# Optimization experiments

Measured on AMD Instinct MI355X. Metric: run time of the kernel, lower is better.

The kernel has to match this reference:

```python
import jax, jax.numpy as jnp
import numpy as np

LEAK = 0.01  # torch F.leaky_relu default slope


def _conv1d(x, W, b):
    # x: [B, Cin, L], W: [Cout, Cin, K] -> [B, Cout, L-K+1]
    y = jax.lax.conv_general_dilated(x, W, window_strides=(1,), padding='VALID',
                                     dimension_numbers=('NCH', 'OIH', 'NCH'))
    return y + b[None, :, None]


def _maxpool3(x):
    # MaxPool1d(kernel=3, stride=3, padding=1); torch pads with -inf
    return jax.lax.reduce_window(x, -jnp.inf, jax.lax.max,
                                 (1, 1, 3), (1, 1, 3),
                                 ((0, 0), (0, 0), (1, 1)))


def _lrelu(x):
    return jnp.where(x >= 0, x, LEAK * x)


def _lstm_layer(x, Wih, Whh, b):
    # x: [B, T, D]; Wih: [4H, D]; Whh: [4H, H]; b: [4H]  (torch gate order i,f,g,o)
    B = x.shape[0]
    H = Whh.shape[1]

    def step(carry, xt):
        h, c = carry
        gates = xt @ Wih.T + h @ Whh.T + b  # [B, 4H]
        i, f, g, o = jnp.split(gates, 4, axis=-1)
        c = jax.nn.sigmoid(f) * c + jax.nn.sigmoid(i) * jnp.tanh(g)
        h = jax.nn.sigmoid(o) * jnp.tanh(c)
        return (h, c), h

    init = (jnp.zeros((B, H), x.dtype), jnp.zeros((B, H), x.dtype))
    _, ys = jax.lax.scan(step, init, jnp.swapaxes(x, 0, 1))
    return jnp.swapaxes(ys, 0, 1)  # [B, T, H]


def _lstm3(x, Wih_s, Whh_s, b_s):
    # 3-layer LSTM (dropout=0 in eval); return h_n[-1] + h_n[-2]
    h_last = []
    for l in range(3):
        x = _lstm_layer(x, Wih_s[l], Whh_s[l], b_s[l])
        h_last.append(x[:, -1])
    return h_last[-1] + h_last[-2]


def _forward(data_in, W1, b1, W2, b2, W3, b3,
             fWih, fWhh, fb, tWih, tWhh, tb,
             L1W, L1b, L2W, L2b, L3W, L3b, L4W, L4b):
    T, F, L, P = data_in.shape
    x = data_in.reshape(T * F, L, P).swapaxes(1, 2)  # [B, 3, L]
    x = _maxpool3(_lrelu(_conv1d(x, W1, b1)))  # [B, 10, 170]
    x = _maxpool3(_lrelu(_conv1d(x, W2, b2)))  # [B, 5, 56]
    x = _maxpool3(_lrelu(_conv1d(x, W3, b3)))  # [B, 10, 18]
    x = x.swapaxes(1, 2)                       # [B, 18, 10] packet vectors
    fv = _lstm3(x, fWih, fWhh, fb)             # [B, 10] flow vectors
    fv = fv.reshape(T, F, -1)                  # [T, F, 10]
    tv = _lstm3(fv, tWih, tWhh, tb)            # [T, 10] trace vectors
    h = _lrelu(tv @ L1W.T + L1b)
    h = _lrelu(h @ L2W.T + L2b)
    h = _lrelu(h @ L3W.T + L3b)
    return h @ L4W.T + L4b                     # [T, 7]


def setup_inputs() -> dict:
    key = jax.random.key(0)
    ks = iter(jax.random.split(key, 32))
    n = lambda shape: jax.random.normal(next(ks), shape, dtype=jnp.float32)
    return {
        'data_in': n((64, 64, 512, 3)),
        'W1': n((10, 3, 5)), 'b1': n((10,)),
        'W2': n((5, 10, 5)), 'b2': n((5,)),
        'W3': n((10, 5, 5)), 'b3': n((10,)),
        'fWih': n((3, 40, 10)), 'fWhh': n((3, 40, 10)), 'fb': n((3, 40)),
        'tWih': n((3, 40, 10)), 'tWhh': n((3, 40, 10)), 'tb': n((3, 40)),
        'L1W': n((128, 10)), 'L1b': n((128,)),
        'L2W': n((256, 128)), 'L2b': n((256,)),
        'L3W': n((64, 256)), 'L3b': n((64,)),
        'L4W': n((7, 64)), 'L4b': n((7,)),
    }


def reference(data_in, W1, b1, W2, b2, W3, b3,
              fWih, fWhh, fb, tWih, tWhh, tb,
              L1W, L1b, L2W, L2b, L3W, L3b, L4W, L4b):
    return _forward(data_in, W1, b1, W2, b2, W3, b3,
                    fWih, fWhh, fb, tWih, tWhh, tb,
                    L1W, L1b, L2W, L2b, L3W, L3b, L4W, L4b)
```

## Files before the change

### kernel.cpp

```cpp
#include <hip/hip_runtime.h>
#include <math.h>

#define LEAK 0.01f

typedef float v2f __attribute__((ext_vector_type(2)));

__device__ __forceinline__ float lrelu(float x) { return fmaxf(x, LEAK * x); }
__device__ __forceinline__ float fast_rcp(float x) { return __builtin_amdgcn_rcpf(x); }
__device__ __forceinline__ float sigmoid_f(float x) {
    return fast_rcp(1.0f + exp2f(-1.44269504f * x));
}
__device__ __forceinline__ float tanh_f(float x) {
    return 2.0f * fast_rcp(1.0f + exp2f(-2.88539008f * x)) - 1.0f;
}
__device__ __forceinline__ float readlane_f(float v, int l) {
    return __int_as_float(__builtin_amdgcn_readlane(__float_as_int(v), l));
}

#define DECL5(p) v2f p##_0, p##_1, p##_2, p##_3, p##_4
#define LOAD5(p, src) do { const v2f* _s5 = (const v2f*)(src); \
    p##_0 = _s5[0]; p##_1 = _s5[1]; p##_2 = _s5[2]; p##_3 = _s5[3]; p##_4 = _s5[4]; } while (0)
#define CP5(d, s) do { d##_0 = s##_0; d##_1 = s##_1; d##_2 = s##_2; d##_3 = s##_3; d##_4 = s##_4; } while (0)
#define ZERO5(p) do { p##_0 = (v2f){0.f,0.f}; p##_1 = (v2f){0.f,0.f}; p##_2 = (v2f){0.f,0.f}; \
    p##_3 = (v2f){0.f,0.f}; p##_4 = (v2f){0.f,0.f}; } while (0)
#define DOT5(w, x) ((w##_0 * x##_0 + w##_1 * x##_1) + (w##_2 * x##_2 + w##_3 * x##_3) + w##_4 * x##_4)

#define DECLU(u) float u##0, u##1, u##2, u##3, u##4, u##5, u##6, u##7, u##8, u##9
#define ZEROU(u) do { u##0=u##1=u##2=u##3=u##4=u##5=u##6=u##7=u##8=u##9=0.0f; } while (0)
#define RL10(u, v) do { \
    u##0 = readlane_f(v, 0); u##1 = readlane_f(v, 1); u##2 = readlane_f(v, 2); \
    u##3 = readlane_f(v, 3); u##4 = readlane_f(v, 4); u##5 = readlane_f(v, 5); \
    u##6 = readlane_f(v, 6); u##7 = readlane_f(v, 7); u##8 = readlane_f(v, 8); \
    u##9 = readlane_f(v, 9); } while (0)
#define DOTU(w, u) (fmaf(w##_0.x, u##0, fmaf(w##_0.y, u##1, fmaf(w##_1.x, u##2, fmaf(w##_1.y, u##3, w##_2.x * u##4)))) \
                  + fmaf(w##_2.y, u##5, fmaf(w##_3.x, u##6, fmaf(w##_3.y, u##7, fmaf(w##_4.x, u##8, w##_4.y * u##9)))))

#define L1C 508
#define L1P 170
#define L2C 166
#define L2P 56
#define L3C 52
#define L3P 18
#define TT 18

__global__ __launch_bounds__(256, 4) void conv_kernel(
    const float* __restrict__ in,
    const float* __restrict__ W1, const float* __restrict__ b1,
    const float* __restrict__ W2, const float* __restrict__ b2,
    const float* __restrict__ W3, const float* __restrict__ b3,
    float* __restrict__ xseq)
{
    __shared__ __align__(16) float xsraw[24 + 1536 + 24];
    __shared__ __align__(16) float y1raw[16 + L1P * 10 + 32];
    __shared__ __align__(16) float y2raw[8 + L2P * 6 + 24];
    float* xs = xsraw + 24;
    float* y1 = y1raw + 16;
    float* y2 = y2raw + 8;

    const int tid = threadIdx.x;
    const int b = blockIdx.x;

    {
        const float4* src = (const float4*)(in + (size_t)b * 1536);
        float4* dst4 = (float4*)xs;
        for (int i = tid; i < 384; i += 256) dst4[i] = src[i];
    }
    __syncthreads();

    {
        const int co = tid % 10;
        const int ob = tid / 10;
        if (tid < 250) {
            float w[15];
            #pragma unroll
            for (int q = 0; q < 15; ++q) w[q] = W1[co * 15 + q];
            const float bias = b1[co];
            const int o0 = ob * 7;
            int sb = 3 * o0 - 1;
            float win[21];
            #pragma unroll
            for (int q = 0; q < 21; ++q) win[q] = xs[3 * sb + q];
            #pragma unroll
            for (int r = 0; r < 7; ++r) {
                const int o = o0 + r;
                if (o < L1P) {
                    float a0 = bias, a1 = bias, a2 = bias;
                    #pragma unroll
                    for (int p = 0; p < 3; ++p) {
                        #pragma unroll
                        for (int k = 0; k < 5; ++k) {
                            const float wv = w[p * 5 + k];
                            a0 = fmaf(wv, win[3 * k + p], a0);
                            a1 = fmaf(wv, win[3 * (k + 1) + p], a1);
                            a2 = fmaf(wv, win[3 * (k + 2) + p], a2);
                        }
                    }
                    float best = -3.0e38f;
                    if (sb >= 0)        best = fmaxf(best, lrelu(a0));
                    best = fmaxf(best, lrelu(a1));
                    if (sb + 2 < L1C)   best = fmaxf(best, lrelu(a2));
                    y1[o * 10 + co] = best;
                }
                if (r < 6 && o + 1 < L1P) {
                    #pragma unroll
                    for (int q = 0; q < 12; ++q) win[q] = win[q + 9];
                    #pragma unroll
                    for (int q = 0; q < 9; ++q) win[12 + q] = xs[3 * sb + 21 + q];
                    sb += 3;
                }
            }
        }
    }
    __syncthreads();

    {
        const int co = tid % 5;
        const int ob = tid / 5;
        v2f wv2[25];
        #pragma unroll
        for (int c2 = 0; c2 < 5; ++c2)
            #pragma unroll
            for (int k = 0; k < 5; ++k)
                wv2[c2 * 5 + k] = (v2f){W2[co * 50 + (2 * c2) * 5 + k],
                                        W2[co * 50 + (2 * c2 + 1) * 5 + k]};
        const float bias = b2[co];
        if (tid < 255) {
            for (int r = 0; r < 2; ++r) {
                const int o = ob + 51 * r;
                if (o < L2P) {
                    const int t0 = 3 * o - 1;
                    v2f v0 = {0.f, 0.f}, v1 = {0.f, 0.f}, v2 = {0.f, 0.f};
                    #pragma unroll
                    for (int m = 0; m < 7; ++m) {
                        v2f rows5[5];
                        const v2f* pr = (const v2f*)(y1 + (t0 + m) * 10);
                        #pragma unroll
                        for (int c2 = 0; c2 < 5; ++c2) rows5[c2] = pr[c2];
                        #pragma unroll
                        for (int c2 = 0; c2 < 5; ++c2) {
                            if (m < 5)            v0 += wv2[c2 * 5 + m] * rows5[c2];
                            if (m >= 1 && m <= 5) v1 += wv2[c2 * 5 + m - 1] * rows5[c2];
                            if (m >= 2)           v2 += wv2[c2 * 5 + m - 2] * rows5[c2];
                        }
                    }
                    const float a0 = bias + v0.x + v0.y;
                    const float a1 = bias + v1.x + v1.y;
                    const float a2 = bias + v2.x + v2.y;
                    float best = -3.0e38f;
                    if (t0 >= 0)        best = fmaxf(best, lrelu(a0));
                    best = fmaxf(best, lrelu(a1));
                    if (t0 + 2 < L2C)   best = fmaxf(best, lrelu(a2));
                    y2[o * 6 + co] = best;
                }
            }
        }
    }
    __syncthreads();

    {
        const int co = tid % 10;
        const int o = tid / 10;
        if (o < L3P) {
            v2f wv3[10];
            float ws3[5];
            #pragma unroll
            for (int c2 = 0; c2 < 2; ++c2)
                #pragma unroll
                for (int k = 0; k < 5; ++k)
                    wv3[c2 * 5 + k] = (v2f){W3[co * 25 + (2 * c2) * 5 + k],
                                            W3[co * 25 + (2 * c2 + 1) * 5 + k]};
            #pragma unroll
            for (int k = 0; k < 5; ++k) ws3[k] = W3[co * 25 + 20 + k];
            const float bias = b3[co];
            const int t0 = 3 * o - 1;
            v2f v0 = {0.f, 0.f}, v1 = {0.f, 0.f}, v2 = {0.f, 0.f};
            float s0 = 0.f, s1 = 0.f, s2 = 0.f;
            #pragma unroll
            for (int m = 0; m < 7; ++m) {
                const float* base = y2 + (t0 + m) * 6;
                v2f ra0 = ((const v2f*)base)[0];
                v2f ra1 = ((const v2f*)base)[1];
                float rcm = base[4];
                if (m < 5) {
                    v0 += wv3[m] * ra0; v0 += wv3[5 + m] * ra1;
                    s0 = fmaf(ws3[m], rcm, s0);
                }
                if (m >= 1 && m <= 5) {
                    v1 += wv3[m - 1] * ra0; v1 += wv3[5 + m - 1] * ra1;
                    s1 = fmaf(ws3[m - 1], rcm, s1);
                }
                if (m >= 2) {
                    v2 += wv3[m - 2] * ra0; v2 += wv3[5 + m - 2] * ra1;
                    s2 = fmaf(ws3[m - 2], rcm, s2);
                }
            }
            const float a0 = bias + s0 + v0.x + v0.y;
            const float a1 = bias + s1 + v1.x + v1.y;
            const float a2 = bias + s2 + v2.x + v2.y;
            float best = -3.0e38f;
            if (t0 >= 0)        best = fmaxf(best, lrelu(a0));
            best = fmaxf(best, lrelu(a1));
            if (t0 + 2 < L3C)   best = fmaxf(best, lrelu(a2));
            xseq[(size_t)b * 180 + o * 10 + co] = best;
        }
    }
}

__global__ __launch_bounds__(256, 2) void flow_lstm_kernel(
    const float* __restrict__ xseq,
    const float* __restrict__ fWih, const float* __restrict__ fWhh,
    const float* __restrict__ fb,
    float* __restrict__ fv)
{
    __shared__ __align__(16) float sbuf[3][16 * 18 * 10];
    const int tid = threadIdx.x;
    const int blk = blockIdx.x;

    {
        const float* src = xseq + (size_t)blk * 2880;
        for (int i = tid; i < 2880; i += 256) sbuf[0][i] = src[i];
    }
    __syncthreads();

    const int el = tid >> 4;
    const int j = tid & 15;
    const int jj = (j < 10) ? j : 0;
    const int base = el * 180;
    const int lane = tid & 63;
    const int gbase = lane & 48;

    float fv_acc = 0.0f;

    for (int l = 0; l < 3; ++l) {
        const float* Wi = fWih + l * 400;
        const float* Wh = fWhh + l * 400;
        const float* bb = fb + l * 40;
        DECL5(wii); DECL5(wif); DECL5(wig); DECL5(wio);
        DECL5(whi); DECL5(whf); DECL5(whg); DECL5(who);
        LOAD5(wii, Wi + jj * 10);
        LOAD5(wif, Wi + (10 + jj) * 10);
        LOAD5(wig, Wi + (20 + jj) * 10);
        LOAD5(wio, Wi + (30 + jj) * 10);
        LOAD5(whi, Wh + jj * 10);
        LOAD5(whf, Wh + (10 + jj) * 10);
        LOAD5(whg, Wh + (20 + jj) * 10);
        LOAD5(who, Wh + (30 + jj) * 10);
        const float bi = bb[jj], bf = bb[10 + jj], bg = bb[20 + jj], bo = bb[30 + jj];

        const float* inb = sbuf[l];
        float* outb = sbuf[(l + 1) % 3];
        float c = 0.0f, hj = 0.0f;
        DECL5(hv); ZERO5(hv);
        DECL5(xc); DECL5(xn);
        LOAD5(xc, inb + base);

        for (int t = 0; t < TT; ++t) {
            if (t + 1 < TT) LOAD5(xn, inb + base + (t + 1) * 10);
            v2f ti_ = DOT5(wii, xc) + DOT5(whi, hv);
            v2f tf_ = DOT5(wif, xc) + DOT5(whf, hv);
            v2f tg_ = DOT5(wig, xc) + DOT5(whg, hv);
            v2f to_ = DOT5(wio, xc) + DOT5(who, hv);
            const float ai = sigmoid_f(bi + ti_.x + ti_.y);
            const float af = sigmoid_f(bf + tf_.x + tf_.y);
            const float ag = tanh_f(bg + tg_.x + tg_.y);
            const float ao = sigmoid_f(bo + to_.x + to_.y);
            c = af * c + ai * ag;
            hj = ao * tanh_f(c);
            if (j < 10) outb[base + t * 10 + j] = hj;
            hv_0 = (v2f){__shfl(hj, gbase + 0), __shfl(hj, gbase + 1)};
            hv_1 = (v2f){__shfl(hj, gbase + 2), __shfl(hj, gbase + 3)};
            hv_2 = (v2f){__shfl(hj, gbase + 4), __shfl(hj, gbase + 5)};
            hv_3 = (v2f){__shfl(hj, gbase + 6), __shfl(hj, gbase + 7)};
            hv_4 = (v2f){__shfl(hj, gbase + 8), __shfl(hj, gbase + 9)};
            CP5(xc, xn);
        }
        if (l >= 1) fv_acc += hj;
        __asm__ __volatile__("" ::: "memory");
    }
    if (j < 10) fv[(size_t)(blk * 16 + el) * 10 + j] = fv_acc;
}

__global__ __launch_bounds__(64, 1) void trace_mlp_kernel(
    const float* __restrict__ fv,
    const float* __restrict__ tWih, const float* __restrict__ tWhh,
    const float* __restrict__ tb,
    const float* __restrict__ L1W, const float* __restrict__ L1b,
    const float* __restrict__ L2W, const float* __restrict__ L2b,
    const float* __restrict__ L3W, const float* __restrict__ L3b,
    const float* __restrict__ L4W, const float* __restrict__ L4b,
    float* __restrict__ out)
{
    __shared__ __align__(16) float xrow[640];
    __shared__ __align__(16) float m1[128];
    __shared__ __align__(16) float m2b[256];
    __shared__ __align__(16) float m3[64];

    const int lane = threadIdx.x;
    const int ti = blockIdx.x;

    {
        const float4* src = (const float4*)(fv + (size_t)ti * 640);
        float4* dst = (float4*)xrow;
        for (int i = lane; i < 160; i += 64) dst[i] = src[i];
    }
    __asm__ __volatile__("" ::: "memory");

    const int gt = lane / 10;
    const bool isg = (gt == 2);
    const float m2g = isg ? 2.0f : 1.0f;
    const float am = isg ? 2.0f : 1.0f;
    const float ab = isg ? -1.0f : 0.0f;

    const int r = (lane < 40) ? lane : 0;
    DECL5(wi0); DECL5(wh0); DECL5(wi1); DECL5(wh1); DECL5(wi2); DECL5(wh2);
    LOAD5(wi0, tWih + r * 10);
    LOAD5(wh0, tWhh + r * 10);
    LOAD5(wi1, tWih + 400 + r * 10);
    LOAD5(wh1, tWhh + 400 + r * 10);
    LOAD5(wi2, tWih + 800 + r * 10);
    LOAD5(wh2, tWhh + 800 + r * 10);
    const float bs0 = tb[r], bs1 = tb[40 + r], bs2 = tb[80 + r];

    DECLU(u0); DECLU(u1); DECLU(u2);
    ZEROU(u0); ZEROU(u1); ZEROU(u2);
    float c0 = 0.0f, c1 = 0.0f, c2 = 0.0f;
    DECL5(xc); DECL5(xn);

#define TICK(D0, D1, D2) do { \
    float g0_ = 0.f, g1_ = 0.f, g2_ = 0.f; \
    if (D2) g2_ = bs2 + DOTU(wi2, u1) + DOTU(wh2, u2); \
    if (D1) g1_ = bs1 + DOTU(wi1, u0) + DOTU(wh1, u1); \
    if (D0) { v2f ax_ = DOT5(wi0, xc); g0_ = bs0 + ax_.x + ax_.y + DOTU(wh0, u0); } \
    float a0_ = 0.f, a1_ = 0.f, a2_ = 0.f; \
    if (D2) a2_ = am * sigmoid_f(m2g * g2_) + ab; \
    if (D1) a1_ = am * sigmoid_f(m2g * g1_) + ab; \
    if (D0) a0_ = am * sigmoid_f(m2g * g0_) + ab; \
    float f2_ = 0.f, q2_ = 0.f, o2_ = 0.f; \
    float f1_ = 0.f, q1_ = 0.f, o1_ = 0.f; \
    float f0_ = 0.f, q0_ = 0.f, o0_ = 0.f; \
    if (D2) { f2_ = __shfl(a2_, lane + 10); q2_ = __shfl(a2_, lane + 20); o2_ = __shfl(a2_, lane + 30); } \
    if (D1) { f1_ = __shfl(a1_, lane + 10); q1_ = __shfl(a1_, lane + 20); o1_ = __shfl(a1_, lane + 30); } \
    if (D0) { f0_ = __shfl(a0_, lane + 10); q0_ = __shfl(a0_, lane + 20); o0_ = __shfl(a0_, lane + 30); } \
    if (D2) { c2 = f2_ * c2 + a2_ * q2_; float h_ = o2_ * tanh_f(c2); RL10(u2, h_); } \
    if (D1) { c1 = f1_ * c1 + a1_ * q1_; float h_ = o1_ * tanh_f(c1); RL10(u1, h_); } \
    if (D0) { c0 = f0_ * c0 + a0_ * q0_; float h_ = o0_ * tanh_f(c0); RL10(u0, h_); } \
} while (0)

    LOAD5(xc, xrow + 0);
    LOAD5(xn, xrow + 10);
    TICK(true, false, false); CP5(xc, xn);
    LOAD5(xn, xrow + 20);
    TICK(true, true, false); CP5(xc, xn);
    for (int tau = 2; tau < 63; ++tau) {
        LOAD5(xn, xrow + (tau + 1) * 10);
        TICK(true, true, true);
        CP5(xc, xn);
    }
    TICK(true, true, true);
    TICK(false, true, true);
    TICK(false, false, true);
#undef TICK

    DECLU(tv);
    tv0 = u10 + u20; tv1 = u11 + u21; tv2 = u12 + u22; tv3 = u13 + u23;
    tv4 = u14 + u24; tv5 = u15 + u25; tv6 = u16 + u26; tv7 = u17 + u27;
    tv8 = u18 + u28; tv9 = u19 + u29;

    {
        DECL5(w1a); DECL5(w1b);
        LOAD5(w1a, L1W + lane * 10);
        LOAD5(w1b, L1W + (lane + 64) * 10);
        float a0 = L1b[lane] + DOTU(w1a, tv);
        float a1 = L1b[lane + 64] + DOTU(w1b, tv);
        m1[lane] = lrelu(a0);
        m1[lane + 64] = lrelu(a1);
    }
    __asm__ __volatile__("" ::: "memory");
    {
        float acc0 = L2b[lane];
        float acc1 = L2b[lane + 64];
        float acc2 = L2b[lane + 128];
        float acc3 = L2b[lane + 192];
        for (int k = 0; k < 128; k += 4) {
            float4 hv = *(const float4*)(m1 + k);
            float4 w0 = *(const float4*)(L2W + (size_t)lane * 128 + k);
            float4 w1 = *(const float4*)(L2W + (size_t)(lane + 64) * 128 + k);
            float4 w2 = *(const float4*)(L2W + (size_t)(lane + 128) * 128 + k);
            float4 w3 = *(const float4*)(L2W + (size_t)(lane + 192) * 128 + k);
            acc0 = fmaf(w0.x, hv.x, acc0); acc0 = fmaf(w0.y, hv.y, acc0);
            acc0 = fmaf(w0.z, hv.z, acc0); acc0 = fmaf(w0.w, hv.w, acc0);
            acc1 = fmaf(w1.x, hv.x, acc1); acc1 = fmaf(w1.y, hv.y, acc1);
            acc1 = fmaf(w1.z, hv.z, acc1); acc1 = fmaf(w1.w, hv.w, acc1);
            acc2 = fmaf(w2.x, hv.x, acc2); acc2 = fmaf(w2.y, hv.y, acc2);
            acc2 = fmaf(w2.z, hv.z, acc2); acc2 = fmaf(w2.w, hv.w, acc2);
            acc3 = fmaf(w3.x, hv.x, acc3); acc3 = fmaf(w3.y, hv.y, acc3);
            acc3 = fmaf(w3.z, hv.z, acc3); acc3 = fmaf(w3.w, hv.w, acc3);
        }
        m2b[lane] = lrelu(acc0);
        m2b[lane + 64] = lrelu(acc1);
        m2b[lane + 128] = lrelu(acc2);
        m2b[lane + 192] = lrelu(acc3);
    }
    __asm__ __volatile__("" ::: "memory");
    {
        float acc = L3b[lane];
        for (int k = 0; k < 256; k += 4) {
            float4 hv = *(const float4*)(m2b + k);
            float4 wv = *(const float4*)(L3W + (size_t)lane * 256 + k);
            acc = fmaf(wv.x, hv.x, acc);
            acc = fmaf(wv.y, hv.y, acc);
            acc = fmaf(wv.z, hv.z, acc);
            acc = fmaf(wv.w, hv.w, acc);
        }
        m3[lane] = lrelu(acc);
    }
    __asm__ __volatile__("" ::: "memory");
    if (lane < 7) {
        float acc = L4b[lane];
        #pragma unroll
        for (int k = 0; k < 64; k += 4) {
            float4 hv = *(const float4*)(m3 + k);
            float4 wv = *(const float4*)(L4W + lane * 64 + k);
            acc = fmaf(wv.x, hv.x, acc);
            acc = fmaf(wv.y, hv.y, acc);
            acc = fmaf(wv.z, hv.z, acc);
            acc = fmaf(wv.w, hv.w, acc);
        }
        out[ti * 7 + lane] = acc;
    }
}

extern "C" void kernel_launch(void* const* d_in, const int* in_sizes, int n_in,
                              void* d_out, int out_size, void* d_ws, size_t ws_size,
                              hipStream_t stream)
{
    const float* data_in = (const float*)d_in[0];
    const float* W1 = (const float*)d_in[1];
    const float* b1 = (const float*)d_in[2];
    const float* W2 = (const float*)d_in[3];
    const float* b2 = (const float*)d_in[4];
    const float* W3 = (const float*)d_in[5];
    const float* b3 = (const float*)d_in[6];
    const float* fWih = (const float*)d_in[7];
    const float* fWhh = (const float*)d_in[8];
    const float* fb = (const float*)d_in[9];
    const float* tWih = (const float*)d_in[10];
    const float* tWhh = (const float*)d_in[11];
    const float* tb = (const float*)d_in[12];
    const float* L1W = (const float*)d_in[13];
    const float* L1b = (const float*)d_in[14];
    const float* L2W = (const float*)d_in[15];
    const float* L2b = (const float*)d_in[16];
    const float* L3W = (const float*)d_in[17];
    const float* L3b = (const float*)d_in[18];
    const float* L4W = (const float*)d_in[19];
    const float* L4b = (const float*)d_in[20];

    float* xseq = (float*)d_ws;
    float* fv = xseq + 4096 * 180;
    float* outp = (float*)d_out;

    conv_kernel<<<4096, 256, 0, stream>>>(data_in, W1, b1, W2, b2, W3, b3, xseq);
    flow_lstm_kernel<<<256, 256, 0, stream>>>(xseq, fWih, fWhh, fb, fv);
    trace_mlp_kernel<<<64, 64, 0, stream>>>(fv, tWih, tWhh, tb,
                                            L1W, L1b, L2W, L2b, L3W, L3b,
                                            L4W, L4b, outp);
}
```

Before: 195.4 us.

## Map trace LSTM layers to lane groups with packed per-unit gate dots

The trace-level 3-layer LSTM wavefront is remapped so each of 30 lanes owns one hidden unit of one layer (layer = lane/10). Each lane computes all four gates with packed v2f FMAs and updates its own cell state, so the per-step gate shuffles go away. A single 30-way readlane broadcast then distributes all three layers' hidden states each tick. This shortens the serial per-step dependency chain of the layer-skewed schedule, at the cost of computing all layers on every tick and masking the inactive ones, plus more weight registers per lane.

```diff
diff --git a/kernel.cpp b/kernel.cpp
--- a/kernel.cpp
+++ b/kernel.cpp
@@ -27,13 +27,22 @@
 
 #define DECLU(u) float u##0, u##1, u##2, u##3, u##4, u##5, u##6, u##7, u##8, u##9
 #define ZEROU(u) do { u##0=u##1=u##2=u##3=u##4=u##5=u##6=u##7=u##8=u##9=0.0f; } while (0)
-#define RL10(u, v) do { \
-    u##0 = readlane_f(v, 0); u##1 = readlane_f(v, 1); u##2 = readlane_f(v, 2); \
-    u##3 = readlane_f(v, 3); u##4 = readlane_f(v, 4); u##5 = readlane_f(v, 5); \
-    u##6 = readlane_f(v, 6); u##7 = readlane_f(v, 7); u##8 = readlane_f(v, 8); \
-    u##9 = readlane_f(v, 9); } while (0)
 #define DOTU(w, u) (fmaf(w##_0.x, u##0, fmaf(w##_0.y, u##1, fmaf(w##_1.x, u##2, fmaf(w##_1.y, u##3, w##_2.x * u##4)))) \
                   + fmaf(w##_2.y, u##5, fmaf(w##_3.x, u##6, fmaf(w##_3.y, u##7, fmaf(w##_4.x, u##8, w##_4.y * u##9)))))
+
+#define DECLW(p) v2f p##0, p##1, p##2, p##3, p##4, p##5, p##6, p##7, p##8, p##9
+#define LOADW_PAIR(p, q0, q1) do { \
+    p##0 = (v2f){(q0)[0], (q1)[0]}; p##1 = (v2f){(q0)[1], (q1)[1]}; \
+    p##2 = (v2f){(q0)[2], (q1)[2]}; p##3 = (v2f){(q0)[3], (q1)[3]}; \
+    p##4 = (v2f){(q0)[4], (q1)[4]}; p##5 = (v2f){(q0)[5], (q1)[5]}; \
+    p##6 = (v2f){(q0)[6], (q1)[6]}; p##7 = (v2f){(q0)[7], (q1)[7]}; \
+    p##8 = (v2f){(q0)[8], (q1)[8]}; p##9 = (v2f){(q0)[9], (q1)[9]}; } while (0)
+#define PKDOT(acc, w, s) do { \
+    acc += w##0 * (v2f){s##0, s##0}; acc += w##1 * (v2f){s##1, s##1}; \
+    acc += w##2 * (v2f){s##2, s##2}; acc += w##3 * (v2f){s##3, s##3}; \
+    acc += w##4 * (v2f){s##4, s##4}; acc += w##5 * (v2f){s##5, s##5}; \
+    acc += w##6 * (v2f){s##6, s##6}; acc += w##7 * (v2f){s##7, s##7}; \
+    acc += w##8 * (v2f){s##8, s##8}; acc += w##9 * (v2f){s##9, s##9}; } while (0)
 
 #define L1C 508
 #define L1P 170
@@ -305,61 +314,83 @@
     }
     __asm__ __volatile__("" ::: "memory");
 
-    const int gt = lane / 10;
-    const bool isg = (gt == 2);
-    const float m2g = isg ? 2.0f : 1.0f;
-    const float am = isg ? 2.0f : 1.0f;
-    const float ab = isg ? -1.0f : 0.0f;
-
-    const int r = (lane < 40) ? lane : 0;
-    DECL5(wi0); DECL5(wh0); DECL5(wi1); DECL5(wh1); DECL5(wi2); DECL5(wh2);
-    LOAD5(wi0, tWih + r * 10);
-    LOAD5(wh0, tWhh + r * 10);
-    LOAD5(wi1, tWih + 400 + r * 10);
-    LOAD5(wh1, tWhh + 400 + r * 10);
-    LOAD5(wi2, tWih + 800 + r * 10);
-    LOAD5(wh2, tWhh + 800 + r * 10);
-    const float bs0 = tb[r], bs1 = tb[40 + r], bs2 = tb[80 + r];
+    const int g = (lane < 30) ? (lane / 10) : 2;
+    const int j = lane % 10;
+
+    const float* WiL = tWih + g * 400;
+    const float* WhL = tWhh + g * 400;
+    const float* bL  = tb + g * 40;
+    DECLW(wxA); DECLW(wxB); DECLW(whA); DECLW(whB);
+    LOADW_PAIR(wxA, WiL + j * 10,        WiL + (10 + j) * 10);
+    LOADW_PAIR(wxB, WiL + (20 + j) * 10, WiL + (30 + j) * 10);
+    LOADW_PAIR(whA, WhL + j * 10,        WhL + (10 + j) * 10);
+    LOADW_PAIR(whB, WhL + (20 + j) * 10, WhL + (30 + j) * 10);
+    const v2f bA = (v2f){bL[j], bL[10 + j]};
+    const v2f bB = (v2f){bL[20 + j], bL[30 + j]};
 
     DECLU(u0); DECLU(u1); DECLU(u2);
     ZEROU(u0); ZEROU(u1); ZEROU(u2);
-    float c0 = 0.0f, c1 = 0.0f, c2 = 0.0f;
+    float c = 0.0f, h = 0.0f;
+    const int tlo = g, thi = 63 + g;
+    const bool g0 = (g == 0), g1 = (g == 1);
+
     DECL5(xc); DECL5(xn);
-
-#define TICK(D0, D1, D2) do { \
-    float g0_ = 0.f, g1_ = 0.f, g2_ = 0.f; \
-    if (D2) g2_ = bs2 + DOTU(wi2, u1) + DOTU(wh2, u2); \
-    if (D1) g1_ = bs1 + DOTU(wi1, u0) + DOTU(wh1, u1); \
-    if (D0) { v2f ax_ = DOT5(wi0, xc); g0_ = bs0 + ax_.x + ax_.y + DOTU(wh0, u0); } \
-    float a0_ = 0.f, a1_ = 0.f, a2_ = 0.f; \
-    if (D2) a2_ = am * sigmoid_f(m2g * g2_) + ab; \
-    if (D1) a1_ = am * sigmoid_f(m2g * g1_) + ab; \
-    if (D0) a0_ = am * sigmoid_f(m2g * g0_) + ab; \
-    float f2_ = 0.f, q2_ = 0.f, o2_ = 0.f; \
-    float f1_ = 0.f, q1_ = 0.f, o1_ = 0.f; \
-    float f0_ = 0.f, q0_ = 0.f, o0_ = 0.f; \
-    if (D2) { f2_ = __shfl(a2_, lane + 10); q2_ = __shfl(a2_, lane + 20); o2_ = __shfl(a2_, lane + 30); } \
-    if (D1) { f1_ = __shfl(a1_, lane + 10); q1_ = __shfl(a1_, lane + 20); o1_ = __shfl(a1_, lane + 30); } \
-    if (D0) { f0_ = __shfl(a0_, lane + 10); q0_ = __shfl(a0_, lane + 20); o0_ = __shfl(a0_, lane + 30); } \
-    if (D2) { c2 = f2_ * c2 + a2_ * q2_; float h_ = o2_ * tanh_f(c2); RL10(u2, h_); } \
-    if (D1) { c1 = f1_ * c1 + a1_ * q1_; float h_ = o1_ * tanh_f(c1); RL10(u1, h_); } \
-    if (D0) { c0 = f0_ * c0 + a0_ * q0_; float h_ = o0_ * tanh_f(c0); RL10(u0, h_); } \
-} while (0)
-
-    LOAD5(xc, xrow + 0);
-    LOAD5(xn, xrow + 10);
-    TICK(true, false, false); CP5(xc, xn);
-    LOAD5(xn, xrow + 20);
-    TICK(true, true, false); CP5(xc, xn);
-    for (int tau = 2; tau < 63; ++tau) {
-        LOAD5(xn, xrow + (tau + 1) * 10);
-        TICK(true, true, true);
+    LOAD5(xc, xrow);
+
+    for (int tau = 0; tau < 66; ++tau) {
+        const int tn = (tau + 1 < 64) ? (tau + 1) : 63;
+        LOAD5(xn, xrow + tn * 10);
+
+        const float in0 = g0 ? xc_0.x : (g1 ? u00 : u10);
+        const float in1 = g0 ? xc_0.y : (g1 ? u01 : u11);
+        const float in2 = g0 ? xc_1.x : (g1 ? u02 : u12);
+        const float in3 = g0 ? xc_1.y : (g1 ? u03 : u13);
+        const float in4 = g0 ? xc_2.x : (g1 ? u04 : u14);
+        const float in5 = g0 ? xc_2.y : (g1 ? u05 : u15);
+        const float in6 = g0 ? xc_3.x : (g1 ? u06 : u16);
+        const float in7 = g0 ? xc_3.y : (g1 ? u07 : u17);
+        const float in8 = g0 ? xc_4.x : (g1 ? u08 : u18);
+        const float in9 = g0 ? xc_4.y : (g1 ? u09 : u19);
+        const float hd0 = g0 ? u00 : (g1 ? u10 : u20);
+        const float hd1 = g0 ? u01 : (g1 ? u11 : u21);
+        const float hd2 = g0 ? u02 : (g1 ? u12 : u22);
+        const float hd3 = g0 ? u03 : (g1 ? u13 : u23);
+        const float hd4 = g0 ? u04 : (g1 ? u14 : u24);
+        const float hd5 = g0 ? u05 : (g1 ? u15 : u25);
+        const float hd6 = g0 ? u06 : (g1 ? u16 : u26);
+        const float hd7 = g0 ? u07 : (g1 ? u17 : u27);
+        const float hd8 = g0 ? u08 : (g1 ? u18 : u28);
+        const float hd9 = g0 ? u09 : (g1 ? u19 : u29);
+
+        v2f gA = bA, gB = bB;
+        PKDOT(gA, wxA, in); PKDOT(gB, wxB, in);
+        PKDOT(gA, whA, hd); PKDOT(gB, whB, hd);
+
+        const float ai = sigmoid_f(gA.x);
+        const float af = sigmoid_f(gA.y);
+        const float ag = tanh_f(gB.x);
+        const float ao = sigmoid_f(gB.y);
+        const float cn = af * c + ai * ag;
+        const float hn = ao * tanh_f(cn);
+        const bool act = (tau >= tlo) && (tau <= thi);
+        c = act ? cn : c;
+        h = act ? hn : h;
+
+        u00 = readlane_f(h, 0); u01 = readlane_f(h, 1); u02 = readlane_f(h, 2);
+        u03 = readlane_f(h, 3); u04 = readlane_f(h, 4); u05 = readlane_f(h, 5);
+        u06 = readlane_f(h, 6); u07 = readlane_f(h, 7); u08 = readlane_f(h, 8);
+        u09 = readlane_f(h, 9);
+        u10 = readlane_f(h, 10); u11 = readlane_f(h, 11); u12 = readlane_f(h, 12);
+        u13 = readlane_f(h, 13); u14 = readlane_f(h, 14); u15 = readlane_f(h, 15);
+        u16 = readlane_f(h, 16); u17 = readlane_f(h, 17); u18 = readlane_f(h, 18);
+        u19 = readlane_f(h, 19);
+        u20 = readlane_f(h, 20); u21 = readlane_f(h, 21); u22 = readlane_f(h, 22);
+        u23 = readlane_f(h, 23); u24 = readlane_f(h, 24); u25 = readlane_f(h, 25);
+        u26 = readlane_f(h, 26); u27 = readlane_f(h, 27); u28 = readlane_f(h, 28);
+        u29 = readlane_f(h, 29);
+
         CP5(xc, xn);
     }
-    TICK(true, true, true);
-    TICK(false, true, true);
-    TICK(false, false, true);
-#undef TICK
 
     DECLU(tv);
     tv0 = u10 + u20; tv1 = u11 + u21; tv2 = u12 + u22; tv3 = u13 + u23;
```

After: 201.2 us. 1.03x slower.
